# Performance work log

Measured on AMD Instinct MI355X. Metric: run time of the kernel, lower is better.

## Reference

```python
import jax, jax.numpy as jnp
import numpy as np
import math

V, T, D_POI, D_OUT = 200000, 512, 256, 512
D_IN = D_POI + 4
D_HID = D_POI + 100


def setup_inputs() -> dict:
    key = jax.random.key(0)
    ks = jax.random.split(key, 12)
    s = 0.02
    return {
        "prev_poi_idx": jax.random.randint(ks[0], (T,), 0, V),
        "prev_time_frac": jax.random.uniform(ks[1], (T,), jnp.float32),
        "poi_final_emb": jax.random.normal(ks[2], (V, D_POI), jnp.float32),
        "poi_latlon_deg": jax.random.uniform(ks[3], (V, 2), jnp.float32) * 90.0,
        "ln_w": jnp.ones((D_IN,), jnp.float32),
        "ln_b": jnp.zeros((D_IN,), jnp.float32),
        "w1": jax.random.normal(ks[4], (D_IN, D_HID), jnp.float32) * s,
        "b1": jnp.zeros((D_HID,), jnp.float32),
        "w2": jax.random.normal(ks[5], (D_HID, D_POI), jnp.float32) * s,
        "b2": jnp.zeros((D_POI,), jnp.float32),
        "w_ih": jax.random.normal(ks[6], (3 * D_OUT, D_POI), jnp.float32) * s,
        "w_hh": jax.random.normal(ks[7], (3 * D_OUT, D_OUT), jnp.float32) * s,
        "b_ih": jnp.zeros((3 * D_OUT,), jnp.float32),
        "b_hh": jnp.zeros((3 * D_OUT,), jnp.float32),
        "q": jax.random.normal(ks[8], (D_OUT,), jnp.float32),
        "log_lam": jnp.array(0.0, jnp.float32),  # log(recency_lambda=1.0)
    }


def _haversine_km(lat1, lon1, lat2, lon2, eps=1e-12):
    dlat = (lat2 - lat1) * 0.5
    dlon = (lon2 - lon1) * 0.5
    a = jnp.sin(dlat) ** 2 + jnp.clip(jnp.cos(lat1), -1, 1) * jnp.clip(jnp.cos(lat2), -1, 1) * jnp.sin(dlon) ** 2
    c = 2.0 * jnp.arctan2(jnp.sqrt(jnp.clip(a, 0, 1)), jnp.sqrt(jnp.clip(1 - a, eps, 1)))
    return 6371.0088 * c


def _forward(prev_poi_idx, prev_time_frac, poi_final_emb, poi_latlon_deg,
             ln_w, ln_b, w1, b1, w2, b2, w_ih, w_hh, b_ih, b_hh, q, log_lam):
    Tn = prev_poi_idx.shape[0]
    poi_emb = poi_final_emb[prev_poi_idx]                       # (T, d_poi)
    t = jnp.clip(prev_time_frac, 0.0, 1.0)
    sin_t = jnp.sin(2.0 * math.pi * t)
    cos_t = jnp.cos(2.0 * math.pi * t)
    dif = jnp.mod(t[1:] - t[:-1], 1.0) * 24.0
    dt_h = jnp.concatenate([jnp.zeros((1,), t.dtype), dif])
    # _poi_radians is under no_grad in torch
    latlon = jax.lax.stop_gradient(poi_latlon_deg[prev_poi_idx])
    lat = jnp.deg2rad(jnp.clip(latlon[:, 0], -90, 90))
    lon = jnp.deg2rad(jnp.clip(latlon[:, 1], -180, 180))
    dd = _haversine_km(lat[:-1], lon[:-1], lat[1:], lon[1:])
    dd_km = jnp.concatenate([jnp.zeros((1,), dd.dtype), dd])
    feat = jnp.stack([sin_t, cos_t, jnp.log1p(dt_h), jnp.log1p(dd_km)], axis=-1)  # (T, 4)
    x = jnp.concatenate([poi_emb, feat], axis=-1)               # (T, d_poi+4)
    # fuse: LayerNorm -> Linear -> GELU -> (Dropout eval=id) -> Linear
    mu = jnp.mean(x, axis=-1, keepdims=True)
    var = jnp.mean((x - mu) ** 2, axis=-1, keepdims=True)
    x = (x - mu) * jax.lax.rsqrt(var + 1e-5) * ln_w + ln_b
    x = jax.nn.gelu(x @ w1 + b1, approximate=False) @ w2 + b2   # (T, d_poi)
    # GRU (single layer, unidirectional), torch gate order r,z,n
    gi_all = x @ w_ih.T + b_ih                                  # (T, 3H)
    def step(h, gi):
        gh = h @ w_hh.T + b_hh
        gi_r, gi_z, gi_n = jnp.split(gi, 3)
        gh_r, gh_z, gh_n = jnp.split(gh, 3)
        r = jax.nn.sigmoid(gi_r + gh_r)
        z = jax.nn.sigmoid(gi_z + gh_z)
        n = jnp.tanh(gi_n + r * gh_n)
        h_new = (1.0 - z) * n + z * h
        return h_new, h_new
    h0 = jnp.zeros((D_OUT,), x.dtype)
    _, hs = jax.lax.scan(step, h0, gi_all)                      # (T, d_out)
    D = hs.shape[-1]
    score = hs @ (q[:D] / jnp.sqrt(jnp.asarray(D, hs.dtype)))
    age = jnp.arange(Tn, dtype=hs.dtype)
    lam = jnp.maximum(jnp.exp(log_lam), 1e-4)
    score = score - lam * (Tn - 1 - age)
    attn = jax.nn.softmax(score, axis=0)
    summary = jnp.sum(attn[:, None] * hs, axis=0, keepdims=True)  # (1, d_out)
    return summary, attn


def reference(prev_poi_idx, prev_time_frac, poi_final_emb, poi_latlon_deg,
              ln_w, ln_b, w1, b1, w2, b2, w_ih, w_hh, b_ih, b_hh, q, log_lam):
    return _forward(prev_poi_idx, prev_time_frac, poi_final_emb, poi_latlon_deg,
                    ln_w, ln_b, w1, b1, w2, b2, w_ih, w_hh, b_ih, b_hh, q, log_lam)
```

## Files before the change

### kernel.cpp

```cpp
#include <hip/hip_runtime.h>
#include <math.h>

#define TT 512
#define DPOI 256
#define DIN 260
#define DHID 356
#define DOUTD 512
#define G3 1536

#define GB 16
#define HU (DOUTD / GB)
#define NRR (3 * HU)
#define NPAY DOUTD

__global__ __launch_bounds__(512)
void pre_kernel(const int* __restrict__ idx, const float* __restrict__ timef,
                const float* __restrict__ latlon, const float* __restrict__ emb,
                const float* __restrict__ lnw, const float* __restrict__ lnb,
                const float* __restrict__ w1, const float* __restrict__ b1,
                const float* __restrict__ w2, const float* __restrict__ b2,
                const float* __restrict__ wih, const float* __restrict__ bih,
                float* __restrict__ gi, unsigned* __restrict__ hcz,
                unsigned* __restrict__ done) {
    int t = blockIdx.x;
    int tid = threadIdx.x;
    int wave = tid >> 6, lane = tid & 63;

    __shared__ float xl[DIN];
    __shared__ float h1l[DHID];
    __shared__ alignas(16) float x2l[DPOI];
    __shared__ float red[8];
    __shared__ float mu_s, rs_s;

    hcz[(size_t)t * 512 + tid] = 0u;
    if (t == 0 && tid < 64) done[tid] = 0u;

    float tv = fminf(fmaxf(timef[t], 0.f), 1.f);
    const float TWO_PI = 6.28318530717958647692f;
    float f0 = sinf(TWO_PI * tv);
    float f1 = cosf(TWO_PI * tv);
    float f2 = 0.f, f3 = 0.f;
    if (t > 0) {
        float tp = fminf(fmaxf(timef[t - 1], 0.f), 1.f);
        float d = tv - tp;
        d = d - floorf(d);
        f2 = log1pf(d * 24.f);
        int i0 = idx[t - 1], i1 = idx[t];
        float la0 = latlon[2 * (size_t)i0], lo0 = latlon[2 * (size_t)i0 + 1];
        float la1 = latlon[2 * (size_t)i1], lo1 = latlon[2 * (size_t)i1 + 1];
        const float D2R = 0.01745329251994329577f;
        float lat1 = fminf(fmaxf(la0, -90.f), 90.f) * D2R;
        float lon1 = fminf(fmaxf(lo0, -180.f), 180.f) * D2R;
        float lat2 = fminf(fmaxf(la1, -90.f), 90.f) * D2R;
        float lon2 = fminf(fmaxf(lo1, -180.f), 180.f) * D2R;
        float dlat = (lat2 - lat1) * 0.5f, dlon = (lon2 - lon1) * 0.5f;
        float sdlat = sinf(dlat), sdlon = sinf(dlon);
        float a = sdlat * sdlat +
                  fminf(fmaxf(cosf(lat1), -1.f), 1.f) * fminf(fmaxf(cosf(lat2), -1.f), 1.f) * sdlon * sdlon;
        float aa = fminf(fmaxf(a, 0.f), 1.f);
        float bb = fminf(fmaxf(1.f - a, 1e-12f), 1.f);
        float cc = 2.f * atan2f(sqrtf(aa), sqrtf(bb));
        f3 = log1pf(6371.0088f * cc);
    }
    float fv = (tid == 0) ? f0 : (tid == 1) ? f1 : (tid == 2) ? f2 : f3;

    float v0 = (tid < 256) ? emb[(size_t)idx[t] * DPOI + tid] : 0.f;
    float v1 = (tid < 4) ? fv : 0.f;

    float s = v0 + v1;
    for (int o = 32; o; o >>= 1) s += __shfl_down(s, o, 64);
    if (lane == 0) red[wave] = s;
    __syncthreads();
    if (tid == 0) {
        float mm = 0.f;
        for (int i = 0; i < 8; ++i) mm += red[i];
        mu_s = mm * (1.f / 260.f);
    }
    __syncthreads();
    float mu = mu_s;
    float d0 = (tid < 256) ? (v0 - mu) : 0.f;
    float d1 = (tid < 4) ? (v1 - mu) : 0.f;
    float sq = d0 * d0 + d1 * d1;
    for (int o = 32; o; o >>= 1) sq += __shfl_down(sq, o, 64);
    __syncthreads();
    if (lane == 0) red[wave] = sq;
    __syncthreads();
    if (tid == 0) {
        float vv = 0.f;
        for (int i = 0; i < 8; ++i) vv += red[i];
        rs_s = rsqrtf(vv * (1.f / 260.f) + 1e-5f);
    }
    __syncthreads();
    float rs = rs_s;
    if (tid < 256) xl[tid] = d0 * rs * lnw[tid] + lnb[tid];
    if (tid < 4)   xl[256 + tid] = d1 * rs * lnw[256 + tid] + lnb[256 + tid];
    __syncthreads();

    if (tid < DHID) {
        float acc = b1[tid];
        #pragma unroll 4
        for (int k = 0; k < DIN; ++k) acc = fmaf(xl[k], w1[k * DHID + tid], acc);
        h1l[tid] = 0.5f * acc * (1.f + erff(acc * 0.70710678118654752440f));
    }
    __syncthreads();

    if (tid < DPOI) {
        float acc = b2[tid];
        #pragma unroll 4
        for (int k = 0; k < DHID; ++k) acc = fmaf(h1l[k], w2[k * DPOI + tid], acc);
        x2l[tid] = acc;
    }
    __syncthreads();

    float4 xv = ((const float4*)x2l)[lane];
    for (int r = wave; r < G3; r += 8) {
        float4 wv = ((const float4*)(wih + (size_t)r * DPOI))[lane];
        float sd = xv.x * wv.x + xv.y * wv.y + xv.z * wv.z + xv.w * wv.w;
        for (int o = 32; o; o >>= 1) sd += __shfl_down(sd, o, 64);
        if (lane == 0) gi[(size_t)t * G3 + r] = sd + bih[r];
    }
}

__global__ __launch_bounds__(1024)
void gru_attn_kernel(const float* __restrict__ gi, const float* __restrict__ whh,
                     const float* __restrict__ bhh, float* __restrict__ hs,
                     unsigned* __restrict__ hcomm, unsigned* __restrict__ done,
                     const float* __restrict__ q, const float* __restrict__ log_lam,
                     float* __restrict__ out) {
    __shared__ alignas(16) float hprev[DOUTD];
    __shared__ float gsum[NRR];
    __shared__ float sc[TT];
    __shared__ float at[TT];
    __shared__ float red[8];
    __shared__ float red2[8];
    __shared__ float denom_s, mx_s;

    int b = blockIdx.x;
    int tid = threadIdx.x;
    int wave = tid >> 6, lane = tid & 63;
    int jbase = b * HU;
    int g2 = lane >> 5, l5 = lane & 31;
    int rr0 = wave * 6 + g2 * 3;

    float4 wf0[4], wf1[4], wf2[4];
    float bl0, bl1, bl2;
    {
        int r0 = rr0, r1 = rr0 + 1, r2 = rr0 + 2;
        const float4* p0 = (const float4*)(whh + (size_t)((r0 >> 5) * DOUTD + jbase + (r0 & 31)) * DOUTD);
        const float4* p1 = (const float4*)(whh + (size_t)((r1 >> 5) * DOUTD + jbase + (r1 & 31)) * DOUTD);
        const float4* p2 = (const float4*)(whh + (size_t)((r2 >> 5) * DOUTD + jbase + (r2 & 31)) * DOUTD);
        #pragma unroll
        for (int m = 0; m < 4; ++m) {
            wf0[m] = p0[m * 32 + l5];
            wf1[m] = p1[m * 32 + l5];
            wf2[m] = p2[m * 32 + l5];
        }
        bl0 = bhh[(r0 >> 5) * DOUTD + jbase + (r0 & 31)];
        bl1 = bhh[(r1 >> 5) * DOUTD + jbase + (r1 & 31)];
        bl2 = bhh[(r2 >> 5) * DOUTD + jbase + (r2 & 31)];
    }
    if (tid < DOUTD) hprev[tid] = 0.f;
    __syncthreads();

    const float4* hp4 = (const float4*)hprev;
    long budget = 3000;

    float gir = 0.f, giz = 0.f, gin = 0.f, hreg = 0.f;
    if (tid < HU) {
        int j = jbase + tid;
        gir = gi[j];
        giz = gi[DOUTD + j];
        gin = gi[2 * DOUTD + j];
    }

    for (int s = 0; s < TT; ++s) {
        unsigned pa = 0, pb2 = 0;
        if (s > 0) {
            bool poller = (wave >= 4 && wave < 12);
            int u = ((wave - 4) << 6) + lane;
            if (poller && (u >> 5) != b) {
                const unsigned* ap = hcomm + (size_t)(s - 1) * NPAY + u;
                unsigned tag = (unsigned)s & 0xffffu;
                asm volatile("global_load_dword %0, %1, off sc0 sc1"
                             : "=v"(pa) : "v"(ap) : "memory");
                float xx = (float)(lane + 1) * 1e-6f;
                #pragma unroll
                for (int qq = 0; qq < 256; ++qq) xx = fmaf(xx, 1.0000002f, 1.1920929e-7f);
                asm volatile("global_load_dword %0, %1, off sc0 sc1"
                             : "=v"(pb2) : "v"(ap), "v"(xx) : "memory");
                do {
                    unsigned tmp; int scnt;
                    asm volatile(
                        "s_movk_i32 %[cnt], 64\n\t"
                        "1:\n\t"
                        "s_waitcnt vmcnt(1)\n\t"
                        "v_and_b32 %[t], 0xffff, %[pa]\n\t"
                        "v_cmp_ne_u32 vcc, %[tag], %[t]\n\t"
                        "s_cbranch_vccz 9f\n\t"
                        "global_load_dword %[pa], %[ptr], off sc0 sc1\n\t"
                        "s_waitcnt vmcnt(1)\n\t"
                        "v_and_b32 %[t], 0xffff, %[pb]\n\t"
                        "v_cmp_ne_u32 vcc, %[tag], %[t]\n\t"
                        "s_cbranch_vccz 8f\n\t"
                        "global_load_dword %[pb], %[ptr], off sc0 sc1\n\t"
                        "s_sub_u32 %[cnt], %[cnt], 1\n\t"
                        "s_cmp_lg_u32 %[cnt], 0\n\t"
                        "s_cbranch_scc1 1b\n\t"
                        "s_branch 9f\n\t"
                        "8:\n\t"
                        "s_waitcnt vmcnt(0)\n\t"
                        "v_mov_b32 %[pa], %[pb]\n\t"
                        "9:\n\t"
                        : [pa]"+v"(pa), [pb]"+v"(pb2), [t]"=&v"(tmp), [cnt]"=&s"(scnt)
                        : [ptr]"v"(ap), [tag]"s"(tag)
                        : "vcc", "scc", "memory");
                    if ((pa & 0xffffu) == tag) break;
                } while (--budget > 0);
                asm volatile("s_waitcnt vmcnt(0)" ::: "memory");
                hprev[u] = __uint_as_float(pa & 0xffff0000u);
            }
            __syncthreads();
            asm volatile("" :: "v"(pa), "v"(pb2));
        }

        float a0 = 0.f, a1 = 0.f, a2 = 0.f;
        #pragma unroll
        for (int m = 0; m < 4; ++m) {
            float4 h4 = hp4[m * 32 + l5];
            a0 = fmaf(wf0[m].x, h4.x, a0); a0 = fmaf(wf0[m].y, h4.y, a0);
            a0 = fmaf(wf0[m].z, h4.z, a0); a0 = fmaf(wf0[m].w, h4.w, a0);
            a1 = fmaf(wf1[m].x, h4.x, a1); a1 = fmaf(wf1[m].y, h4.y, a1);
            a1 = fmaf(wf1[m].z, h4.z, a1); a1 = fmaf(wf1[m].w, h4.w, a1);
            a2 = fmaf(wf2[m].x, h4.x, a2); a2 = fmaf(wf2[m].y, h4.y, a2);
            a2 = fmaf(wf2[m].z, h4.z, a2); a2 = fmaf(wf2[m].w, h4.w, a2);
        }
        #pragma unroll
        for (int o = 1; o < 32; o <<= 1) {
            a0 += __shfl_xor(a0, o, 64);
            a1 += __shfl_xor(a1, o, 64);
            a2 += __shfl_xor(a2, o, 64);
        }
        if (l5 == 0) {
            gsum[rr0]     = a0 + bl0;
            gsum[rr0 + 1] = a1 + bl1;
            gsum[rr0 + 2] = a2 + bl2;
        }
        __syncthreads();

        if (tid < HU) {
            float gr  = gir + gsum[tid];
            float gz  = giz + gsum[HU + tid];
            float ghn = gsum[2 * HU + tid];
            float r = __builtin_amdgcn_rcpf(1.f + __expf(-gr));
            float z = __builtin_amdgcn_rcpf(1.f + __expf(-gz));
            float xt = gin + r * ghn;
            float n = 1.f - 2.f * __builtin_amdgcn_rcpf(__expf(2.f * xt) + 1.f);
            float hn = (1.f - z) * n + z * hreg;
            hreg = hn;
            unsigned ub = __float_as_uint(hn);
            ub += 0x7fffu + ((ub >> 16) & 1u);
            unsigned pay = (ub & 0xffff0000u) | ((unsigned)(s + 1) & 0xffffu);
            __hip_atomic_store(&hcomm[(size_t)s * NPAY + jbase + tid], pay,
                               __ATOMIC_RELAXED, __HIP_MEMORY_SCOPE_AGENT);
            int j = jbase + tid;
            __hip_atomic_store(&hs[(size_t)s * DOUTD + j], hn,
                               __ATOMIC_RELAXED, __HIP_MEMORY_SCOPE_AGENT);
            hprev[j] = hn;
            if (s + 1 < TT) {
                const float* gn = gi + (size_t)(s + 1) * G3;
                gir = gn[j]; giz = gn[DOUTD + j]; gin = gn[2 * DOUTD + j];
            }
        }
    }

    asm volatile("s_waitcnt vmcnt(0)" ::: "memory");
    __syncthreads();
    if (tid == 0)
        __hip_atomic_store(&done[b], 1u, __ATOMIC_RELAXED, __HIP_MEMORY_SCOPE_AGENT);
    if (b != 0) return;

    {
        long dbud = 20L * 1000 * 1000;
        if (tid < GB) {
            while (__hip_atomic_load(&done[tid], __ATOMIC_RELAXED,
                                     __HIP_MEMORY_SCOPE_AGENT) == 0u) {
                if (--dbud < 0) break;
            }
        }
        __syncthreads();
    }

    const float qscale = 0.04419417382415921757f;
    for (int r = wave; r < TT; r += 16) {
        float acc = 0.f;
        #pragma unroll
        for (int m = 0; m < 8; ++m) {
            int k = lane + 64 * m;
            acc = fmaf(hs[(size_t)r * DOUTD + k], q[k], acc);
        }
        for (int o = 32; o; o >>= 1) acc += __shfl_down(acc, o, 64);
        if (lane == 0) sc[r] = acc * qscale;
    }
    __syncthreads();
    float lam = fmaxf(expf(log_lam[0]), 1e-4f);
    float s_i = (tid < TT) ? (sc[tid] - lam * (float)(TT - 1 - tid)) : -1e30f;

    float mval = s_i;
    for (int o = 32; o; o >>= 1) mval = fmaxf(mval, __shfl_down(mval, o, 64));
    if (lane == 0 && wave < 8) red[wave] = mval;
    __syncthreads();
    if (tid == 0) {
        float mm = red[0];
        for (int i = 1; i < 8; ++i) mm = fmaxf(mm, red[i]);
        mx_s = mm;
    }
    __syncthreads();
    float e = (tid < TT) ? expf(s_i - mx_s) : 0.f;
    float ssum = e;
    for (int o = 32; o; o >>= 1) ssum += __shfl_down(ssum, o, 64);
    if (lane == 0 && wave < 8) red2[wave] = ssum;
    __syncthreads();
    if (tid == 0) {
        float dsum = 0.f;
        for (int i = 0; i < 8; ++i) dsum += red2[i];
        denom_s = dsum;
    }
    __syncthreads();
    if (tid < TT) {
        float attn = e / denom_s;
        out[DOUTD + tid] = attn;
        at[tid] = attn;
    }
    __syncthreads();
    if (tid < TT) {
        float acc = 0.f;
        for (int i = 0; i < TT; ++i) acc = fmaf(at[i], hs[(size_t)i * DOUTD + tid], acc);
        out[tid] = acc;
    }
}

extern "C" void kernel_launch(void* const* d_in, const int* in_sizes, int n_in,
                              void* d_out, int out_size, void* d_ws, size_t ws_size,
                              hipStream_t stream) {
    const int*   idx    = (const int*)d_in[0];
    const float* timef  = (const float*)d_in[1];
    const float* emb    = (const float*)d_in[2];
    const float* latlon = (const float*)d_in[3];
    const float* lnw    = (const float*)d_in[4];
    const float* lnb    = (const float*)d_in[5];
    const float* w1     = (const float*)d_in[6];
    const float* b1     = (const float*)d_in[7];
    const float* w2     = (const float*)d_in[8];
    const float* b2     = (const float*)d_in[9];
    const float* wih    = (const float*)d_in[10];
    const float* whh    = (const float*)d_in[11];
    const float* bih    = (const float*)d_in[12];
    const float* bhh    = (const float*)d_in[13];
    const float* q      = (const float*)d_in[14];
    const float* loglam = (const float*)d_in[15];
    float* out = (float*)d_out;

    unsigned* hcomm = (unsigned*)d_ws;
    unsigned* done  = hcomm + (size_t)TT * NPAY;
    float* gi = (float*)(done + 64);
    float* hs = gi + (size_t)TT * G3;

    pre_kernel<<<TT, 512, 0, stream>>>(idx, timef, latlon, emb, lnw, lnb,
                                       w1, b1, w2, b2, wih, bih, gi, hcomm, done);
    gru_attn_kernel<<<GB, 1024, 0, stream>>>(gi, whh, bhh, hs, hcomm, done,
                                             q, loglam, out);
}
```

Baseline: 1.541 ms.

## Fuse preprocessing into GRU kernel and overlap via per-timestep ready flags

The pre-kernel and the GRU recurrence kernel are merged into one launch. The extra 256 blocks each compute the input projection for two timesteps and publish a ready flag per timestep. The 16 GRU blocks poll those flags and prefetch gi into a shared ring buffer, so the recurrence can start before all projections finish. Zeroing of the flags and communication buffers moves to a separate init kernel. The recurrent matvec is also regrouped from 6 rows per wave over 16 waves to 8 rows per wave over 12 waves, freeing waves 13 and 14 for polling and prefetch. This depends on the GRU blocks being co-resident with the producer blocks and adds spin-wait cost on the critical path.

Result: slower. 1.635 ms (+6.1%).

```diff
diff --git a/kernel.cpp b/kernel.cpp
--- a/kernel.cpp
+++ b/kernel.cpp
@@ -12,123 +12,144 @@
 #define HU (DOUTD / GB)
 #define NRR (3 * HU)
 #define NPAY DOUTD
-
-__global__ __launch_bounds__(512)
-void pre_kernel(const int* __restrict__ idx, const float* __restrict__ timef,
-                const float* __restrict__ latlon, const float* __restrict__ emb,
-                const float* __restrict__ lnw, const float* __restrict__ lnb,
-                const float* __restrict__ w1, const float* __restrict__ b1,
-                const float* __restrict__ w2, const float* __restrict__ b2,
-                const float* __restrict__ wih, const float* __restrict__ bih,
-                float* __restrict__ gi, unsigned* __restrict__ hcz,
-                unsigned* __restrict__ done) {
-    int t = blockIdx.x;
+#define PREB 256
+#define NZ4 ((TT * NPAY + TT + 64) / 4)
+
+__global__ void init_kernel(uint4* __restrict__ p) {
+    int i = blockIdx.x * blockDim.x + threadIdx.x;
+    int stride = gridDim.x * blockDim.x;
+    uint4 z; z.x = 0u; z.y = 0u; z.z = 0u; z.w = 0u;
+    for (; i < NZ4; i += stride) p[i] = z;
+}
+
+__global__ __launch_bounds__(1024)
+void mega_kernel(const int* __restrict__ idx, const float* __restrict__ timef,
+                 const float* __restrict__ latlon, const float* __restrict__ emb,
+                 const float* __restrict__ lnw, const float* __restrict__ lnb,
+                 const float* __restrict__ w1, const float* __restrict__ b1,
+                 const float* __restrict__ w2, const float* __restrict__ b2,
+                 const float* __restrict__ wih, const float* __restrict__ bih,
+                 const float* __restrict__ whh, const float* __restrict__ bhh,
+                 float* __restrict__ gi, float* __restrict__ hs,
+                 unsigned* __restrict__ hcomm, unsigned* __restrict__ ready,
+                 unsigned* __restrict__ done,
+                 const float* __restrict__ q, const float* __restrict__ log_lam,
+                 float* __restrict__ out) {
     int tid = threadIdx.x;
     int wave = tid >> 6, lane = tid & 63;
 
-    __shared__ float xl[DIN];
-    __shared__ float h1l[DHID];
-    __shared__ alignas(16) float x2l[DPOI];
-    __shared__ float red[8];
-    __shared__ float mu_s, rs_s;
-
-    hcz[(size_t)t * 512 + tid] = 0u;
-    if (t == 0 && tid < 64) done[tid] = 0u;
-
-    float tv = fminf(fmaxf(timef[t], 0.f), 1.f);
-    const float TWO_PI = 6.28318530717958647692f;
-    float f0 = sinf(TWO_PI * tv);
-    float f1 = cosf(TWO_PI * tv);
-    float f2 = 0.f, f3 = 0.f;
-    if (t > 0) {
-        float tp = fminf(fmaxf(timef[t - 1], 0.f), 1.f);
-        float d = tv - tp;
-        d = d - floorf(d);
-        f2 = log1pf(d * 24.f);
-        int i0 = idx[t - 1], i1 = idx[t];
-        float la0 = latlon[2 * (size_t)i0], lo0 = latlon[2 * (size_t)i0 + 1];
-        float la1 = latlon[2 * (size_t)i1], lo1 = latlon[2 * (size_t)i1 + 1];
-        const float D2R = 0.01745329251994329577f;
-        float lat1 = fminf(fmaxf(la0, -90.f), 90.f) * D2R;
-        float lon1 = fminf(fmaxf(lo0, -180.f), 180.f) * D2R;
-        float lat2 = fminf(fmaxf(la1, -90.f), 90.f) * D2R;
-        float lon2 = fminf(fmaxf(lo1, -180.f), 180.f) * D2R;
-        float dlat = (lat2 - lat1) * 0.5f, dlon = (lon2 - lon1) * 0.5f;
-        float sdlat = sinf(dlat), sdlon = sinf(dlon);
-        float a = sdlat * sdlat +
-                  fminf(fmaxf(cosf(lat1), -1.f), 1.f) * fminf(fmaxf(cosf(lat2), -1.f), 1.f) * sdlon * sdlon;
-        float aa = fminf(fmaxf(a, 0.f), 1.f);
-        float bb = fminf(fmaxf(1.f - a, 1e-12f), 1.f);
-        float cc = 2.f * atan2f(sqrtf(aa), sqrtf(bb));
-        f3 = log1pf(6371.0088f * cc);
-    }
-    float fv = (tid == 0) ? f0 : (tid == 1) ? f1 : (tid == 2) ? f2 : f3;
-
-    float v0 = (tid < 256) ? emb[(size_t)idx[t] * DPOI + tid] : 0.f;
-    float v1 = (tid < 4) ? fv : 0.f;
-
-    float s = v0 + v1;
-    for (int o = 32; o; o >>= 1) s += __shfl_down(s, o, 64);
-    if (lane == 0) red[wave] = s;
-    __syncthreads();
-    if (tid == 0) {
-        float mm = 0.f;
-        for (int i = 0; i < 8; ++i) mm += red[i];
-        mu_s = mm * (1.f / 260.f);
-    }
-    __syncthreads();
-    float mu = mu_s;
-    float d0 = (tid < 256) ? (v0 - mu) : 0.f;
-    float d1 = (tid < 4) ? (v1 - mu) : 0.f;
-    float sq = d0 * d0 + d1 * d1;
-    for (int o = 32; o; o >>= 1) sq += __shfl_down(sq, o, 64);
-    __syncthreads();
-    if (lane == 0) red[wave] = sq;
-    __syncthreads();
-    if (tid == 0) {
-        float vv = 0.f;
-        for (int i = 0; i < 8; ++i) vv += red[i];
-        rs_s = rsqrtf(vv * (1.f / 260.f) + 1e-5f);
-    }
-    __syncthreads();
-    float rs = rs_s;
-    if (tid < 256) xl[tid] = d0 * rs * lnw[tid] + lnb[tid];
-    if (tid < 4)   xl[256 + tid] = d1 * rs * lnw[256 + tid] + lnb[256 + tid];
-    __syncthreads();
-
-    if (tid < DHID) {
-        float acc = b1[tid];
-        #pragma unroll 4
-        for (int k = 0; k < DIN; ++k) acc = fmaf(xl[k], w1[k * DHID + tid], acc);
-        h1l[tid] = 0.5f * acc * (1.f + erff(acc * 0.70710678118654752440f));
-    }
-    __syncthreads();
-
-    if (tid < DPOI) {
-        float acc = b2[tid];
-        #pragma unroll 4
-        for (int k = 0; k < DHID; ++k) acc = fmaf(h1l[k], w2[k * DPOI + tid], acc);
-        x2l[tid] = acc;
-    }
-    __syncthreads();
-
-    float4 xv = ((const float4*)x2l)[lane];
-    for (int r = wave; r < G3; r += 8) {
-        float4 wv = ((const float4*)(wih + (size_t)r * DPOI))[lane];
-        float sd = xv.x * wv.x + xv.y * wv.y + xv.z * wv.z + xv.w * wv.w;
-        for (int o = 32; o; o >>= 1) sd += __shfl_down(sd, o, 64);
-        if (lane == 0) gi[(size_t)t * G3 + r] = sd + bih[r];
-    }
-}
-
-__global__ __launch_bounds__(1024)
-void gru_attn_kernel(const float* __restrict__ gi, const float* __restrict__ whh,
-                     const float* __restrict__ bhh, float* __restrict__ hs,
-                     unsigned* __restrict__ hcomm, unsigned* __restrict__ done,
-                     const float* __restrict__ q, const float* __restrict__ log_lam,
-                     float* __restrict__ out) {
+    if (blockIdx.x >= GB) {
+        __shared__ float xl[DIN];
+        __shared__ float h1l[DHID];
+        __shared__ alignas(16) float x2l[DPOI];
+        __shared__ float red16[16];
+        __shared__ float mu_s, rs_s;
+        int pb = blockIdx.x - GB;
+
+        for (int half = 0; half < 2; ++half) {
+            int t = pb * 2 + half;
+
+            float fv = 0.f;
+            if (tid < 4) {
+                float tv = fminf(fmaxf(timef[t], 0.f), 1.f);
+                const float TWO_PI = 6.28318530717958647692f;
+                float f0 = sinf(TWO_PI * tv);
+                float f1 = cosf(TWO_PI * tv);
+                float f2 = 0.f, f3 = 0.f;
+                if (t > 0) {
+                    float tp = fminf(fmaxf(timef[t - 1], 0.f), 1.f);
+                    float d = tv - tp;
+                    d = d - floorf(d);
+                    f2 = log1pf(d * 24.f);
+                    int i0 = idx[t - 1], i1 = idx[t];
+                    float la0 = latlon[2 * (size_t)i0], lo0 = latlon[2 * (size_t)i0 + 1];
+                    float la1 = latlon[2 * (size_t)i1], lo1 = latlon[2 * (size_t)i1 + 1];
+                    const float D2R = 0.01745329251994329577f;
+                    float lat1 = fminf(fmaxf(la0, -90.f), 90.f) * D2R;
+                    float lon1 = fminf(fmaxf(lo0, -180.f), 180.f) * D2R;
+                    float lat2 = fminf(fmaxf(la1, -90.f), 90.f) * D2R;
+                    float lon2 = fminf(fmaxf(lo1, -180.f), 180.f) * D2R;
+                    float dlat = (lat2 - lat1) * 0.5f, dlon = (lon2 - lon1) * 0.5f;
+                    float sdlat = sinf(dlat), sdlon = sinf(dlon);
+                    float a = sdlat * sdlat +
+                              fminf(fmaxf(cosf(lat1), -1.f), 1.f) * fminf(fmaxf(cosf(lat2), -1.f), 1.f) * sdlon * sdlon;
+                    float aa = fminf(fmaxf(a, 0.f), 1.f);
+                    float bb = fminf(fmaxf(1.f - a, 1e-12f), 1.f);
+                    float cc = 2.f * atan2f(sqrtf(aa), sqrtf(bb));
+                    f3 = log1pf(6371.0088f * cc);
+                }
+                fv = (tid == 0) ? f0 : (tid == 1) ? f1 : (tid == 2) ? f2 : f3;
+            }
+
+            float v0 = (tid < 256) ? emb[(size_t)idx[t] * DPOI + tid] : 0.f;
+            float v1 = (tid < 4) ? fv : 0.f;
+
+            float s = v0 + v1;
+            for (int o = 32; o; o >>= 1) s += __shfl_down(s, o, 64);
+            if (lane == 0) red16[wave] = s;
+            __syncthreads();
+            if (tid == 0) {
+                float mm = 0.f;
+                for (int i = 0; i < 16; ++i) mm += red16[i];
+                mu_s = mm * (1.f / 260.f);
+            }
+            __syncthreads();
+            float mu = mu_s;
+            float d0 = (tid < 256) ? (v0 - mu) : 0.f;
+            float d1 = (tid < 4) ? (v1 - mu) : 0.f;
+            float sq = d0 * d0 + d1 * d1;
+            for (int o = 32; o; o >>= 1) sq += __shfl_down(sq, o, 64);
+            __syncthreads();
+            if (lane == 0) red16[wave] = sq;
+            __syncthreads();
+            if (tid == 0) {
+                float vv = 0.f;
+                for (int i = 0; i < 16; ++i) vv += red16[i];
+                rs_s = rsqrtf(vv * (1.f / 260.f) + 1e-5f);
+            }
+            __syncthreads();
+            float rs = rs_s;
+            if (tid < 256) xl[tid] = d0 * rs * lnw[tid] + lnb[tid];
+            if (tid < 4)   xl[256 + tid] = d1 * rs * lnw[256 + tid] + lnb[256 + tid];
+            __syncthreads();
+
+            if (tid < DHID) {
+                float acc = b1[tid];
+                #pragma unroll 4
+                for (int k = 0; k < DIN; ++k) acc = fmaf(xl[k], w1[k * DHID + tid], acc);
+                h1l[tid] = 0.5f * acc * (1.f + erff(acc * 0.70710678118654752440f));
+            }
+            __syncthreads();
+
+            if (tid < DPOI) {
+                float acc = b2[tid];
+                #pragma unroll 4
+                for (int k = 0; k < DHID; ++k) acc = fmaf(h1l[k], w2[k * DPOI + tid], acc);
+                x2l[tid] = acc;
+            }
+            __syncthreads();
+
+            float4 xv = ((const float4*)x2l)[lane];
+            for (int r = wave; r < G3; r += 16) {
+                float4 wv = ((const float4*)(wih + (size_t)r * DPOI))[lane];
+                float sd = xv.x * wv.x + xv.y * wv.y + xv.z * wv.z + xv.w * wv.w;
+                for (int o = 32; o; o >>= 1) sd += __shfl_down(sd, o, 64);
+                if (lane == 0)
+                    __hip_atomic_store(&gi[(size_t)t * G3 + r], sd + bih[r],
+                                       __ATOMIC_RELAXED, __HIP_MEMORY_SCOPE_AGENT);
+            }
+            __syncthreads();
+            if (tid == 0)
+                __hip_atomic_store(&ready[t], 1u, __ATOMIC_RELAXED,
+                                   __HIP_MEMORY_SCOPE_AGENT);
+            __syncthreads();
+        }
+        return;
+    }
+
     __shared__ alignas(16) float hprev[DOUTD];
     __shared__ float gsum[NRR];
+    __shared__ float gibuf[4][3][HU];
     __shared__ float sc[TT];
     __shared__ float at[TT];
     __shared__ float red[8];
@@ -136,42 +157,61 @@
     __shared__ float denom_s, mx_s;
 
     int b = blockIdx.x;
-    int tid = threadIdx.x;
-    int wave = tid >> 6, lane = tid & 63;
     int jbase = b * HU;
     int g2 = lane >> 5, l5 = lane & 31;
-    int rr0 = wave * 6 + g2 * 3;
-
-    float4 wf0[4], wf1[4], wf2[4];
-    float bl0, bl1, bl2;
-    {
-        int r0 = rr0, r1 = rr0 + 1, r2 = rr0 + 2;
-        const float4* p0 = (const float4*)(whh + (size_t)((r0 >> 5) * DOUTD + jbase + (r0 & 31)) * DOUTD);
-        const float4* p1 = (const float4*)(whh + (size_t)((r1 >> 5) * DOUTD + jbase + (r1 & 31)) * DOUTD);
-        const float4* p2 = (const float4*)(whh + (size_t)((r2 >> 5) * DOUTD + jbase + (r2 & 31)) * DOUTD);
+    int rr0 = wave * 8 + g2 * 4;
+
+    float4 wr0[4], wr1[4], wr2[4], wr3[4];
+    float br0 = 0.f, br1 = 0.f, br2 = 0.f, br3 = 0.f;
+    if (wave < 12) {
+        const float4* p0 = (const float4*)(whh + (size_t)(((rr0 + 0) >> 5) * DOUTD + jbase + ((rr0 + 0) & 31)) * DOUTD);
+        const float4* p1 = (const float4*)(whh + (size_t)(((rr0 + 1) >> 5) * DOUTD + jbase + ((rr0 + 1) & 31)) * DOUTD);
+        const float4* p2 = (const float4*)(whh + (size_t)(((rr0 + 2) >> 5) * DOUTD + jbase + ((rr0 + 2) & 31)) * DOUTD);
+        const float4* p3 = (const float4*)(whh + (size_t)(((rr0 + 3) >> 5) * DOUTD + jbase + ((rr0 + 3) & 31)) * DOUTD);
         #pragma unroll
         for (int m = 0; m < 4; ++m) {
-            wf0[m] = p0[m * 32 + l5];
-            wf1[m] = p1[m * 32 + l5];
-            wf2[m] = p2[m * 32 + l5];
-        }
-        bl0 = bhh[(r0 >> 5) * DOUTD + jbase + (r0 & 31)];
-        bl1 = bhh[(r1 >> 5) * DOUTD + jbase + (r1 & 31)];
-        bl2 = bhh[(r2 >> 5) * DOUTD + jbase + (r2 & 31)];
+            wr0[m] = p0[m * 32 + l5];
+            wr1[m] = p1[m * 32 + l5];
+            wr2[m] = p2[m * 32 + l5];
+            wr3[m] = p3[m * 32 + l5];
+        }
+        br0 = bhh[((rr0 + 0) >> 5) * DOUTD + jbase + ((rr0 + 0) & 31)];
+        br1 = bhh[((rr0 + 1) >> 5) * DOUTD + jbase + ((rr0 + 1) & 31)];
+        br2 = bhh[((rr0 + 2) >> 5) * DOUTD + jbase + ((rr0 + 2) & 31)];
+        br3 = bhh[((rr0 + 3) >> 5) * DOUTD + jbase + ((rr0 + 3) & 31)];
     }
     if (tid < DOUTD) hprev[tid] = 0.f;
-    __syncthreads();
+
+    long budget = 3000;
+    long rbudget = 2000000;
+
+    if (wave == 13 && lane < 3) {
+        while (__hip_atomic_load(&ready[lane], __ATOMIC_RELAXED,
+                                 __HIP_MEMORY_SCOPE_AGENT) == 0u) {
+            if (--rbudget < 0) break;
+        }
+    }
+    __syncthreads();
+
+    if (wave == 14 && lane < HU) {
+        for (int tt = 0; tt < 2; ++tt) {
+            const float* gp = gi + (size_t)tt * G3 + jbase + lane;
+            unsigned u0, u1, u2;
+            asm volatile("global_load_dword %0, %3, off sc0 sc1\n\t"
+                         "global_load_dword %1, %4, off sc0 sc1\n\t"
+                         "global_load_dword %2, %5, off sc0 sc1\n\t"
+                         "s_waitcnt vmcnt(0)"
+                         : "=&v"(u0), "=&v"(u1), "=&v"(u2)
+                         : "v"(gp), "v"(gp + DOUTD), "v"(gp + 2 * DOUTD)
+                         : "memory");
+            gibuf[tt][0][lane] = __uint_as_float(u0);
+            gibuf[tt][1][lane] = __uint_as_float(u1);
+            gibuf[tt][2][lane] = __uint_as_float(u2);
+        }
+    }
 
     const float4* hp4 = (const float4*)hprev;
-    long budget = 3000;
-
-    float gir = 0.f, giz = 0.f, gin = 0.f, hreg = 0.f;
-    if (tid < HU) {
-        int j = jbase + tid;
-        gir = gi[j];
-        giz = gi[DOUTD + j];
-        gin = gi[2 * DOUTD + j];
-    }
+    float hreg = 0.f;
 
     for (int s = 0; s < TT; ++s) {
         unsigned pa = 0, pb2 = 0;
@@ -219,35 +259,65 @@
                 asm volatile("s_waitcnt vmcnt(0)" ::: "memory");
                 hprev[u] = __uint_as_float(pa & 0xffff0000u);
             }
+            if (wave == 13 && lane == 0 && s + 2 < TT) {
+                while (__hip_atomic_load(&ready[s + 2], __ATOMIC_RELAXED,
+                                         __HIP_MEMORY_SCOPE_AGENT) == 0u) {
+                    if (--rbudget < 0) break;
+                }
+            }
+            if (wave == 14 && lane < HU && s + 1 < TT) {
+                const float* gp = gi + (size_t)(s + 1) * G3 + jbase + lane;
+                unsigned u0, u1, u2;
+                asm volatile("global_load_dword %0, %3, off sc0 sc1\n\t"
+                             "global_load_dword %1, %4, off sc0 sc1\n\t"
+                             "global_load_dword %2, %5, off sc0 sc1\n\t"
+                             "s_waitcnt vmcnt(0)"
+                             : "=&v"(u0), "=&v"(u1), "=&v"(u2)
+                             : "v"(gp), "v"(gp + DOUTD), "v"(gp + 2 * DOUTD)
+                             : "memory");
+                int bi = (s + 1) & 3;
+                gibuf[bi][0][lane] = __uint_as_float(u0);
+                gibuf[bi][1][lane] = __uint_as_float(u1);
+                gibuf[bi][2][lane] = __uint_as_float(u2);
+            }
             __syncthreads();
             asm volatile("" :: "v"(pa), "v"(pb2));
         }
 
-        float a0 = 0.f, a1 = 0.f, a2 = 0.f;
-        #pragma unroll
-        for (int m = 0; m < 4; ++m) {
-            float4 h4 = hp4[m * 32 + l5];
-            a0 = fmaf(wf0[m].x, h4.x, a0); a0 = fmaf(wf0[m].y, h4.y, a0);
-            a0 = fmaf(wf0[m].z, h4.z, a0); a0 = fmaf(wf0[m].w, h4.w, a0);
-            a1 = fmaf(wf1[m].x, h4.x, a1); a1 = fmaf(wf1[m].y, h4.y, a1);
-            a1 = fmaf(wf1[m].z, h4.z, a1); a1 = fmaf(wf1[m].w, h4.w, a1);
-            a2 = fmaf(wf2[m].x, h4.x, a2); a2 = fmaf(wf2[m].y, h4.y, a2);
-            a2 = fmaf(wf2[m].z, h4.z, a2); a2 = fmaf(wf2[m].w, h4.w, a2);
-        }
-        #pragma unroll
-        for (int o = 1; o < 32; o <<= 1) {
-            a0 += __shfl_xor(a0, o, 64);
-            a1 += __shfl_xor(a1, o, 64);
-            a2 += __shfl_xor(a2, o, 64);
-        }
-        if (l5 == 0) {
-            gsum[rr0]     = a0 + bl0;
-            gsum[rr0 + 1] = a1 + bl1;
-            gsum[rr0 + 2] = a2 + bl2;
+        if (wave < 12) {
+            float a0 = 0.f, a1 = 0.f, a2 = 0.f, a3 = 0.f;
+            #pragma unroll
+            for (int m = 0; m < 4; ++m) {
+                float4 h4 = hp4[m * 32 + l5];
+                a0 = fmaf(wr0[m].x, h4.x, a0); a0 = fmaf(wr0[m].y, h4.y, a0);
+                a0 = fmaf(wr0[m].z, h4.z, a0); a0 = fmaf(wr0[m].w, h4.w, a0);
+                a1 = fmaf(wr1[m].x, h4.x, a1); a1 = fmaf(wr1[m].y, h4.y, a1);
+                a1 = fmaf(wr1[m].z, h4.z, a1); a1 = fmaf(wr1[m].w, h4.w, a1);
+                a2 = fmaf(wr2[m].x, h4.x, a2); a2 = fmaf(wr2[m].y, h4.y, a2);
+                a2 = fmaf(wr2[m].z, h4.z, a2); a2 = fmaf(wr2[m].w, h4.w, a2);
+                a3 = fmaf(wr3[m].x, h4.x, a3); a3 = fmaf(wr3[m].y, h4.y, a3);
+                a3 = fmaf(wr3[m].z, h4.z, a3); a3 = fmaf(wr3[m].w, h4.w, a3);
+            }
+            #pragma unroll
+            for (int o = 1; o < 32; o <<= 1) {
+                a0 += __shfl_xor(a0, o, 64);
+                a1 += __shfl_xor(a1, o, 64);
+                a2 += __shfl_xor(a2, o, 64);
+                a3 += __shfl_xor(a3, o, 64);
+            }
+            if (l5 == 0) {
+                gsum[rr0]     = a0 + br0;
+                gsum[rr0 + 1] = a1 + br1;
+                gsum[rr0 + 2] = a2 + br2;
+                gsum[rr0 + 3] = a3 + br3;
+            }
         }
         __syncthreads();
 
         if (tid < HU) {
+            float gir = gibuf[s & 3][0][tid];
+            float giz = gibuf[s & 3][1][tid];
+            float gin = gibuf[s & 3][2][tid];
             float gr  = gir + gsum[tid];
             float gz  = giz + gsum[HU + tid];
             float ghn = gsum[2 * HU + tid];
@@ -266,10 +336,6 @@
             __hip_atomic_store(&hs[(size_t)s * DOUTD + j], hn,
                                __ATOMIC_RELAXED, __HIP_MEMORY_SCOPE_AGENT);
             hprev[j] = hn;
-            if (s + 1 < TT) {
-                const float* gn = gi + (size_t)(s + 1) * G3;
-                gir = gn[j]; giz = gn[DOUTD + j]; gin = gn[2 * DOUTD + j];
-            }
         }
     }
 
@@ -361,12 +427,14 @@
     float* out = (float*)d_out;
 
     unsigned* hcomm = (unsigned*)d_ws;
-    unsigned* done  = hcomm + (size_t)TT * NPAY;
+    unsigned* ready = hcomm + (size_t)TT * NPAY;
+    unsigned* done  = ready + TT;
     float* gi = (float*)(done + 64);
     float* hs = gi + (size_t)TT * G3;
 
-    pre_kernel<<<TT, 512, 0, stream>>>(idx, timef, latlon, emb, lnw, lnb,
-                                       w1, b1, w2, b2, wih, bih, gi, hcomm, done);
-    gru_attn_kernel<<<GB, 1024, 0, stream>>>(gi, whh, bhh, hs, hcomm, done,
-                                             q, loglam, out);
+    init_kernel<<<256, 256, 0, stream>>>((uint4*)d_ws);
+    mega_kernel<<<GB + PREB, 1024, 0, stream>>>(idx, timef, latlon, emb, lnw, lnb,
+                                                w1, b1, w2, b2, wih, bih, whh, bhh,
+                                                gi, hs, hcomm, ready, done,
+                                                q, loglam, out);
 }
```

## Batch four timesteps per block in pre_kernel to reuse weight loads

Applied to the files above, without the earlier changes.

The pre-processing kernel now handles four timesteps per block, so 128 blocks run instead of 512. Each weight element of w1, w2 and w_ih is loaded once and applied to four activation vectors, which cuts global weight traffic by a factor of four. The trig features are computed only by the four threads that use them. In exchange the grid is smaller, register use per thread is higher, and layernorm runs serially over the four timesteps.

After: 1.577 ms. 2.4% more time.

```diff
diff --git a/kernel.cpp b/kernel.cpp
--- a/kernel.cpp
+++ b/kernel.cpp
@@ -12,6 +12,8 @@
 #define HU (DOUTD / GB)
 #define NRR (3 * HU)
 #define NPAY DOUTD
+#define PBLK 128
+#define TPB 4
 
 __global__ __launch_bounds__(512)
 void pre_kernel(const int* __restrict__ idx, const float* __restrict__ timef,
@@ -22,102 +24,144 @@
                 const float* __restrict__ wih, const float* __restrict__ bih,
                 float* __restrict__ gi, unsigned* __restrict__ hcz,
                 unsigned* __restrict__ done) {
-    int t = blockIdx.x;
+    int p = blockIdx.x;
+    int t0 = p * TPB;
     int tid = threadIdx.x;
     int wave = tid >> 6, lane = tid & 63;
 
-    __shared__ float xl[DIN];
-    __shared__ float h1l[DHID];
-    __shared__ alignas(16) float x2l[DPOI];
+    __shared__ float xl4[TPB][DIN];
+    __shared__ float h14[TPB][DHID];
+    __shared__ alignas(16) float x24[TPB][DPOI];
     __shared__ float red[8];
     __shared__ float mu_s, rs_s;
 
-    hcz[(size_t)t * 512 + tid] = 0u;
-    if (t == 0 && tid < 64) done[tid] = 0u;
-
-    float tv = fminf(fmaxf(timef[t], 0.f), 1.f);
-    const float TWO_PI = 6.28318530717958647692f;
-    float f0 = sinf(TWO_PI * tv);
-    float f1 = cosf(TWO_PI * tv);
-    float f2 = 0.f, f3 = 0.f;
-    if (t > 0) {
-        float tp = fminf(fmaxf(timef[t - 1], 0.f), 1.f);
-        float d = tv - tp;
-        d = d - floorf(d);
-        f2 = log1pf(d * 24.f);
-        int i0 = idx[t - 1], i1 = idx[t];
-        float la0 = latlon[2 * (size_t)i0], lo0 = latlon[2 * (size_t)i0 + 1];
-        float la1 = latlon[2 * (size_t)i1], lo1 = latlon[2 * (size_t)i1 + 1];
-        const float D2R = 0.01745329251994329577f;
-        float lat1 = fminf(fmaxf(la0, -90.f), 90.f) * D2R;
-        float lon1 = fminf(fmaxf(lo0, -180.f), 180.f) * D2R;
-        float lat2 = fminf(fmaxf(la1, -90.f), 90.f) * D2R;
-        float lon2 = fminf(fmaxf(lo1, -180.f), 180.f) * D2R;
-        float dlat = (lat2 - lat1) * 0.5f, dlon = (lon2 - lon1) * 0.5f;
-        float sdlat = sinf(dlat), sdlon = sinf(dlon);
-        float a = sdlat * sdlat +
-                  fminf(fmaxf(cosf(lat1), -1.f), 1.f) * fminf(fmaxf(cosf(lat2), -1.f), 1.f) * sdlon * sdlon;
-        float aa = fminf(fmaxf(a, 0.f), 1.f);
-        float bb = fminf(fmaxf(1.f - a, 1e-12f), 1.f);
-        float cc = 2.f * atan2f(sqrtf(aa), sqrtf(bb));
-        f3 = log1pf(6371.0088f * cc);
-    }
-    float fv = (tid == 0) ? f0 : (tid == 1) ? f1 : (tid == 2) ? f2 : f3;
-
-    float v0 = (tid < 256) ? emb[(size_t)idx[t] * DPOI + tid] : 0.f;
-    float v1 = (tid < 4) ? fv : 0.f;
-
-    float s = v0 + v1;
-    for (int o = 32; o; o >>= 1) s += __shfl_down(s, o, 64);
-    if (lane == 0) red[wave] = s;
-    __syncthreads();
-    if (tid == 0) {
-        float mm = 0.f;
-        for (int i = 0; i < 8; ++i) mm += red[i];
-        mu_s = mm * (1.f / 260.f);
-    }
-    __syncthreads();
-    float mu = mu_s;
-    float d0 = (tid < 256) ? (v0 - mu) : 0.f;
-    float d1 = (tid < 4) ? (v1 - mu) : 0.f;
-    float sq = d0 * d0 + d1 * d1;
-    for (int o = 32; o; o >>= 1) sq += __shfl_down(sq, o, 64);
-    __syncthreads();
-    if (lane == 0) red[wave] = sq;
-    __syncthreads();
-    if (tid == 0) {
-        float vv = 0.f;
-        for (int i = 0; i < 8; ++i) vv += red[i];
-        rs_s = rsqrtf(vv * (1.f / 260.f) + 1e-5f);
-    }
-    __syncthreads();
-    float rs = rs_s;
-    if (tid < 256) xl[tid] = d0 * rs * lnw[tid] + lnb[tid];
-    if (tid < 4)   xl[256 + tid] = d1 * rs * lnw[256 + tid] + lnb[256 + tid];
+    for (int i = tid; i < 2048; i += 512) hcz[(size_t)p * 2048 + i] = 0u;
+    if (p == 0 && tid < 64) done[tid] = 0u;
+
+    for (int tt = 0; tt < TPB; ++tt) {
+        int t = t0 + tt;
+        float fv = 0.f;
+        if (tid < 4) {
+            float tv = fminf(fmaxf(timef[t], 0.f), 1.f);
+            const float TWO_PI = 6.28318530717958647692f;
+            float f0 = sinf(TWO_PI * tv);
+            float f1 = cosf(TWO_PI * tv);
+            float f2 = 0.f, f3 = 0.f;
+            if (t > 0) {
+                float tp = fminf(fmaxf(timef[t - 1], 0.f), 1.f);
+                float d = tv - tp;
+                d = d - floorf(d);
+                f2 = log1pf(d * 24.f);
+                int i0 = idx[t - 1], i1 = idx[t];
+                float la0 = latlon[2 * (size_t)i0], lo0 = latlon[2 * (size_t)i0 + 1];
+                float la1 = latlon[2 * (size_t)i1], lo1 = latlon[2 * (size_t)i1 + 1];
+                const float D2R = 0.01745329251994329577f;
+                float lat1 = fminf(fmaxf(la0, -90.f), 90.f) * D2R;
+                float lon1 = fminf(fmaxf(lo0, -180.f), 180.f) * D2R;
+                float lat2 = fminf(fmaxf(la1, -90.f), 90.f) * D2R;
+                float lon2 = fminf(fmaxf(lo1, -180.f), 180.f) * D2R;
+                float dlat = (lat2 - lat1) * 0.5f, dlon = (lon2 - lon1) * 0.5f;
+                float sdlat = sinf(dlat), sdlon = sinf(dlon);
+                float a = sdlat * sdlat +
+                          fminf(fmaxf(cosf(lat1), -1.f), 1.f) * fminf(fmaxf(cosf(lat2), -1.f), 1.f) * sdlon * sdlon;
+                float aa = fminf(fmaxf(a, 0.f), 1.f);
+                float bb = fminf(fmaxf(1.f - a, 1e-12f), 1.f);
+                float cc = 2.f * atan2f(sqrtf(aa), sqrtf(bb));
+                f3 = log1pf(6371.0088f * cc);
+            }
+            fv = (tid == 0) ? f0 : (tid == 1) ? f1 : (tid == 2) ? f2 : f3;
+        }
+
+        float v0 = (tid < 256) ? emb[(size_t)idx[t] * DPOI + tid] : 0.f;
+        float v1 = (tid < 4) ? fv : 0.f;
+
+        float s = v0 + v1;
+        for (int o = 32; o; o >>= 1) s += __shfl_down(s, o, 64);
+        if (lane == 0) red[wave] = s;
+        __syncthreads();
+        if (tid == 0) {
+            float mm = 0.f;
+            for (int i = 0; i < 8; ++i) mm += red[i];
+            mu_s = mm * (1.f / 260.f);
+        }
+        __syncthreads();
+        float mu = mu_s;
+        float d0 = (tid < 256) ? (v0 - mu) : 0.f;
+        float d1 = (tid < 4) ? (v1 - mu) : 0.f;
+        float sq = d0 * d0 + d1 * d1;
+        for (int o = 32; o; o >>= 1) sq += __shfl_down(sq, o, 64);
+        __syncthreads();
+        if (lane == 0) red[wave] = sq;
+        __syncthreads();
+        if (tid == 0) {
+            float vv = 0.f;
+            for (int i = 0; i < 8; ++i) vv += red[i];
+            rs_s = rsqrtf(vv * (1.f / 260.f) + 1e-5f);
+        }
+        __syncthreads();
+        float rs = rs_s;
+        if (tid < 256) xl4[tt][tid] = d0 * rs * lnw[tid] + lnb[tid];
+        if (tid < 4)   xl4[tt][256 + tid] = d1 * rs * lnw[256 + tid] + lnb[256 + tid];
+    }
     __syncthreads();
 
     if (tid < DHID) {
-        float acc = b1[tid];
+        float bb = b1[tid];
+        float a0 = bb, a1 = bb, a2 = bb, a3 = bb;
         #pragma unroll 4
-        for (int k = 0; k < DIN; ++k) acc = fmaf(xl[k], w1[k * DHID + tid], acc);
-        h1l[tid] = 0.5f * acc * (1.f + erff(acc * 0.70710678118654752440f));
+        for (int k = 0; k < DIN; ++k) {
+            float w = w1[k * DHID + tid];
+            a0 = fmaf(xl4[0][k], w, a0);
+            a1 = fmaf(xl4[1][k], w, a1);
+            a2 = fmaf(xl4[2][k], w, a2);
+            a3 = fmaf(xl4[3][k], w, a3);
+        }
+        const float IS2 = 0.70710678118654752440f;
+        h14[0][tid] = 0.5f * a0 * (1.f + erff(a0 * IS2));
+        h14[1][tid] = 0.5f * a1 * (1.f + erff(a1 * IS2));
+        h14[2][tid] = 0.5f * a2 * (1.f + erff(a2 * IS2));
+        h14[3][tid] = 0.5f * a3 * (1.f + erff(a3 * IS2));
     }
     __syncthreads();
 
     if (tid < DPOI) {
-        float acc = b2[tid];
+        float bb = b2[tid];
+        float a0 = bb, a1 = bb, a2 = bb, a3 = bb;
         #pragma unroll 4
-        for (int k = 0; k < DHID; ++k) acc = fmaf(h1l[k], w2[k * DPOI + tid], acc);
-        x2l[tid] = acc;
-    }
-    __syncthreads();
-
-    float4 xv = ((const float4*)x2l)[lane];
+        for (int k = 0; k < DHID; ++k) {
+            float w = w2[k * DPOI + tid];
+            a0 = fmaf(h14[0][k], w, a0);
+            a1 = fmaf(h14[1][k], w, a1);
+            a2 = fmaf(h14[2][k], w, a2);
+            a3 = fmaf(h14[3][k], w, a3);
+        }
+        x24[0][tid] = a0; x24[1][tid] = a1; x24[2][tid] = a2; x24[3][tid] = a3;
+    }
+    __syncthreads();
+
+    float4 xv0 = ((const float4*)x24[0])[lane];
+    float4 xv1 = ((const float4*)x24[1])[lane];
+    float4 xv2 = ((const float4*)x24[2])[lane];
+    float4 xv3 = ((const float4*)x24[3])[lane];
     for (int r = wave; r < G3; r += 8) {
         float4 wv = ((const float4*)(wih + (size_t)r * DPOI))[lane];
-        float sd = xv.x * wv.x + xv.y * wv.y + xv.z * wv.z + xv.w * wv.w;
-        for (int o = 32; o; o >>= 1) sd += __shfl_down(sd, o, 64);
-        if (lane == 0) gi[(size_t)t * G3 + r] = sd + bih[r];
+        float s0 = wv.x * xv0.x + wv.y * xv0.y + wv.z * xv0.z + wv.w * xv0.w;
+        float s1 = wv.x * xv1.x + wv.y * xv1.y + wv.z * xv1.z + wv.w * xv1.w;
+        float s2 = wv.x * xv2.x + wv.y * xv2.y + wv.z * xv2.z + wv.w * xv2.w;
+        float s3 = wv.x * xv3.x + wv.y * xv3.y + wv.z * xv3.z + wv.w * xv3.w;
+        for (int o = 32; o; o >>= 1) {
+            s0 += __shfl_down(s0, o, 64);
+            s1 += __shfl_down(s1, o, 64);
+            s2 += __shfl_down(s2, o, 64);
+            s3 += __shfl_down(s3, o, 64);
+        }
+        if (lane == 0) {
+            float bb = bih[r];
+            gi[(size_t)(t0 + 0) * G3 + r] = s0 + bb;
+            gi[(size_t)(t0 + 1) * G3 + r] = s1 + bb;
+            gi[(size_t)(t0 + 2) * G3 + r] = s2 + bb;
+            gi[(size_t)(t0 + 3) * G3 + r] = s3 + bb;
+        }
     }
 }
 
@@ -365,8 +409,8 @@
     float* gi = (float*)(done + 64);
     float* hs = gi + (size_t)TT * G3;
 
-    pre_kernel<<<TT, 512, 0, stream>>>(idx, timef, latlon, emb, lnw, lnb,
-                                       w1, b1, w2, b2, wih, bih, gi, hcomm, done);
+    pre_kernel<<<PBLK, 512, 0, stream>>>(idx, timef, latlon, emb, lnw, lnb,
+                                         w1, b1, w2, b2, wih, bih, gi, hcomm, done);
     gru_attn_kernel<<<GB, 1024, 0, stream>>>(gi, whh, bhh, hs, hcomm, done,
                                              q, loglam, out);
 }
```
